# Kernel optimization log

Measured on AMD Instinct MI355X. Metric: run time of the kernel, lower is better.

The kernel has to match this reference:

```python
import jax, jax.numpy as jnp
import numpy as np
import math

LOG2PI = math.log(2 * math.pi)
K = 16           # num_comp
C = 64           # channels
S, NN, T = 2, 207, 12
NFEAT = S * NN * T  # 4968 = in_features of the Conv1d(k=1) projections


def setup_inputs() -> dict:
    key = jax.random.key(0)
    ks = jax.random.split(key, 7)
    x = jax.random.normal(ks[0], (8, C, S, NN, T), dtype=jnp.float32)
    scale = 0.02
    alpha_w = jax.random.normal(ks[1], (K, NFEAT), dtype=jnp.float32) * scale
    alpha_b = jax.random.normal(ks[2], (K,), dtype=jnp.float32) * scale
    sigma_w = jax.random.normal(ks[3], (K, NFEAT), dtype=jnp.float32) * scale
    sigma_b = jax.random.normal(ks[4], (K,), dtype=jnp.float32) * scale
    mu_w = jax.random.normal(ks[5], (K, NFEAT), dtype=jnp.float32) * scale
    mu_b = jax.random.normal(ks[6], (K,), dtype=jnp.float32) * scale
    return {"x": x, "alpha_w": alpha_w, "alpha_b": alpha_b,
            "sigma_w": sigma_w, "sigma_b": sigma_b, "mu_w": mu_w, "mu_b": mu_b}


def reference(x, alpha_w, alpha_b, sigma_w, sigma_b, mu_w, mu_b):
    b, c, s, n, t = x.shape
    hd = x.reshape(b, c, -1)                       # (b, c, N); torch's hd after final permute
    # Conv1d(kernel=1) over the (b, N, c) layout == per-(b,c) linear N -> K
    def proj(w, bias):
        return jnp.einsum('bcn,kn->bck', hd, w) + bias  # (b, c, K)
    alphas = jax.nn.softmax(proj(alpha_w, alpha_b), axis=-1)   # softmax over K
    sigma = jnp.exp(proj(sigma_w, sigma_b))                    # (b, c, K)
    mu = proj(mu_w, mu_b)                                      # (b, c, K)

    # log N(h | mu_k, sigma_k^2): (b, c, N, K) via broadcasting (original repeats)
    z = (hd[..., None] - mu[:, :, None, :]) / sigma[:, :, None, :]
    log_component_prob = -jnp.log(sigma)[:, :, None, :] - 0.5 * LOG2PI - 0.5 * z * z
    log_prob = log_component_prob + jnp.log(alphas)[:, :, None, :]
    # original computes log(sum(exp(.))) without max-subtraction; replicate exactly
    log_sum = jnp.log(jnp.sum(jnp.exp(log_prob), axis=-1, keepdims=True))
    weightedlogPdf = log_prob - log_sum                        # (b, c, N, K)
    labels = jnp.argmax(weightedlogPdf, axis=-1)               # (b, c, N) int

    # cluster_norm: due to torch aliasing (new_mu = new_sigma = labels, same storage),
    # both end up equal to sigma gathered by label, so norm uses sigma_g for center+scale.
    sigma_g = jnp.take_along_axis(sigma, labels, axis=2)       # (b, c, N)
    norm = (hd - sigma_g) / (sigma_g + 1e-5)
    out = norm.reshape(b, c, s, n, t)

    # probability regularization loss
    first_item = jnp.mean(jnp.exp(weightedlogPdf) * log_component_prob)
    q_z = jnp.mean(weightedlogPdf, axis=2)                     # (b, c, K)
    kl = jnp.mean(alphas * (jnp.log(alphas) - q_z))            # F.kl_div(q_z, alphas, 'mean')
    loss = kl - first_item
    return out, loss
```

## Files before the change

kernel.cpp:

```cpp
#include <hip/hip_runtime.h>
#include <math.h>

#define NROWS 512
#define NFEAT 4968
#define NVEC4 1242
#define HALF_LOG2PI 0.91893853320467274178032973640562

__global__ __launch_bounds__(256) void proj_kernel(
    const float* __restrict__ x,
    const float* __restrict__ aw,
    const float* __restrict__ sw,
    const float* __restrict__ mw,
    double* __restrict__ proj)
{
    const int jgroup = blockIdx.x >> 9;
    const int row    = blockIdx.x & 511;
    const int t = threadIdx.x;
    const int j = t >> 4;
    const int s = t & 15;

    const float* W = (jgroup == 0) ? aw : (jgroup == 1) ? sw : mw;
    const float4* xp = (const float4*)(x + (size_t)row * NFEAT);
    const float4* wp = (const float4*)(W + (size_t)j * NFEAT);

    double a0 = 0.0, a1 = 0.0, a2 = 0.0, a3 = 0.0;
    #pragma unroll 4
    for (int i = s; i < NVEC4; i += 16) {
        float4 xv = xp[i], wv = wp[i];
        a0 = fma((double)xv.x, (double)wv.x, a0);
        a1 = fma((double)xv.y, (double)wv.y, a1);
        a2 = fma((double)xv.z, (double)wv.z, a2);
        a3 = fma((double)xv.w, (double)wv.w, a3);
    }
    double a = (a0 + a1) + (a2 + a3);

    #pragma unroll
    for (int off = 8; off; off >>= 1) a += __shfl_xor(a, off, 16);

    if (s == 0)
        proj[(size_t)row * 48 + jgroup * 16 + j] = a;
}

__global__ __launch_bounds__(256) void gmm_kernel(
    const float* __restrict__ x,
    const double* __restrict__ proj,
    const float* __restrict__ ab,
    const float* __restrict__ sb,
    const float* __restrict__ mb,
    float* __restrict__ out,
    float* __restrict__ part_kl,
    float* __restrict__ part_fi)
{
    const int row = blockIdx.x;
    const int tid = threadIdx.x;

    __shared__ double mu_s[16], isg_s[16], cl_s[16];
    __shared__ double sig_s[16], ivp_s[16];
    __shared__ float  la_s[16], al_s[16];
    __shared__ float  red[4][18];
    __shared__ float  tot_s[18];
    __shared__ float  kl_s[16];

    if (tid < 16) {
        int k = tid;
        double pa = proj[row * 48 + k]      + (double)ab[k];
        double ps = proj[row * 48 + 16 + k] + (double)sb[k];
        double pm = proj[row * 48 + 32 + k] + (double)mb[k];

        double m = pa;
        #pragma unroll
        for (int off = 8; off; off >>= 1) m = fmax(m, __shfl_xor(m, off, 16));
        double e = exp(pa - m);
        double ss = e;
        #pragma unroll
        for (int off = 8; off; off >>= 1) ss += __shfl_xor(ss, off, 16);
        double alpha = e / ss;
        double la = log(alpha);

        double sg  = exp(ps);
        double lsg = log(sg);

        mu_s[k]  = pm;
        isg_s[k] = 1.0 / sg;
        cl_s[k]  = la - lsg - HALF_LOG2PI;
        sig_s[k] = sg;
        ivp_s[k] = 1.0 / (sg + 1e-5);
        la_s[k]  = (float)la;
        al_s[k]  = (float)alpha;
    }
    __syncthreads();

    double mu_r[16], isg_r[16], cl_r[16];
    float  la_r[16];
    #pragma unroll
    for (int k = 0; k < 16; ++k) {
        mu_r[k] = mu_s[k]; isg_r[k] = isg_s[k];
        cl_r[k] = cl_s[k]; la_r[k] = la_s[k];
    }

    float S1[16];
    #pragma unroll
    for (int k = 0; k < 16; ++k) S1[k] = 0.f;
    float S2 = 0.f;
    float FI = 0.f;

    const float* xr = x + (size_t)row * NFEAT;
    float* outr = out + (size_t)row * NFEAT;

    for (int n = tid; n < NFEAT; n += 256) {
        double h = (double)xr[n];
        double maxlp = -1.0e300;
        int lab = 0;
        float sumexp = 0.f, s1 = 0.f;
        #pragma unroll
        for (int k = 0; k < 16; ++k) {
            double z  = (h - mu_r[k]) * isg_r[k];
            double lp = fma(z * z, -0.5, cl_r[k]);
            if (lp > maxlp) { maxlp = lp; lab = k; }
            float lpf = (float)lp;
            float e   = __expf(lpf);
            float lcp = lpf - la_r[k];
            sumexp += e;
            s1 = fmaf(e, lcp, s1);
            S1[k] += lcp;
        }
        S2 += __logf(sumexp);
        FI += s1 / sumexp;

        double sg = sig_s[lab];
        outr[n] = (float)((h - sg) * ivp_s[lab]);
    }

    float vals[18];
    #pragma unroll
    for (int i = 0; i < 16; ++i) vals[i] = S1[i];
    vals[16] = S2; vals[17] = FI;

    #pragma unroll
    for (int i = 0; i < 18; ++i) {
        float v = vals[i];
        #pragma unroll
        for (int off = 32; off; off >>= 1) v += __shfl_xor(v, off, 64);
        vals[i] = v;
    }
    const int wave = tid >> 6, lane = tid & 63;
    if (lane == 0) {
        #pragma unroll
        for (int i = 0; i < 18; ++i) red[wave][i] = vals[i];
    }
    __syncthreads();
    if (tid < 18)
        tot_s[tid] = red[0][tid] + red[1][tid] + red[2][tid] + red[3][tid];
    __syncthreads();
    if (tid < 16) {
        const float invN = 1.0f / (float)NFEAT;
        float q = tot_s[tid] * invN + la_s[tid] - tot_s[16] * invN;
        kl_s[tid] = al_s[tid] * (la_s[tid] - q);
    }
    __syncthreads();
    if (tid == 0) {
        float kacc = 0.f;
        #pragma unroll
        for (int i = 0; i < 16; ++i) kacc += kl_s[i];
        part_kl[row] = kacc;
        part_fi[row] = tot_s[17];
    }
}

__global__ __launch_bounds__(256) void loss_kernel(
    const float* __restrict__ part_kl,
    const float* __restrict__ part_fi,
    float* __restrict__ loss_out)
{
    const int tid = threadIdx.x;
    double a = 0.0, b = 0.0;
    for (int i = tid; i < NROWS; i += 256) {
        a += (double)part_kl[i];
        b += (double)part_fi[i];
    }
    #pragma unroll
    for (int off = 32; off; off >>= 1) {
        a += __shfl_xor(a, off, 64);
        b += __shfl_xor(b, off, 64);
    }
    __shared__ double ra[4], rb[4];
    const int wave = tid >> 6, lane = tid & 63;
    if (lane == 0) { ra[wave] = a; rb[wave] = b; }
    __syncthreads();
    if (tid == 0) {
        double ka = ra[0] + ra[1] + ra[2] + ra[3];
        double kb = rb[0] + rb[1] + rb[2] + rb[3];
        loss_out[0] = (float)(ka / 8192.0 - kb / 40697856.0);
    }
}

extern "C" void kernel_launch(void* const* d_in, const int* in_sizes, int n_in,
                              void* d_out, int out_size, void* d_ws, size_t ws_size,
                              hipStream_t stream) {
    const float* x  = (const float*)d_in[0];
    const float* aw = (const float*)d_in[1];
    const float* ab = (const float*)d_in[2];
    const float* sw = (const float*)d_in[3];
    const float* sb = (const float*)d_in[4];
    const float* mw = (const float*)d_in[5];
    const float* mb = (const float*)d_in[6];
    float* out = (float*)d_out;

    double* proj   = (double*)d_ws;
    float* part_kl = (float*)(proj + NROWS * 48);
    float* part_fi = part_kl + NROWS;

    proj_kernel<<<3 * NROWS, 256, 0, stream>>>(x, aw, sw, mw, proj);
    gmm_kernel<<<NROWS, 256, 0, stream>>>(x, proj, ab, sb, mb, out, part_kl, part_fi);
    loss_kernel<<<1, 256, 0, stream>>>(part_kl, part_fi, out + (size_t)NROWS * NFEAT);
}
```

Before: 62.55 us.

## Tile projection over rows and K-slices, split GMM rows across blocks

```diff
diff --git a/kernel.cpp b/kernel.cpp
--- a/kernel.cpp
+++ b/kernel.cpp
@@ -4,6 +4,9 @@
 #define NROWS 512
 #define NFEAT 4968
 #define NVEC4 1242
+#define KSLICES 6
+#define SLICE4 207
+#define GSL 1242
 #define HALF_LOG2PI 0.91893853320467274178032973640562
 
 __global__ __launch_bounds__(256) void proj_kernel(
@@ -11,82 +14,110 @@
     const float* __restrict__ aw,
     const float* __restrict__ sw,
     const float* __restrict__ mw,
-    double* __restrict__ proj)
-{
-    const int jgroup = blockIdx.x >> 9;
-    const int row    = blockIdx.x & 511;
+    double* __restrict__ pp)
+{
+    const int rowtile = blockIdx.x & 63;
+    const int jg      = (blockIdx.x >> 6) % 3;
+    const int sl      = blockIdx.x / 192;
     const int t = threadIdx.x;
     const int j = t >> 4;
-    const int s = t & 15;
-
-    const float* W = (jgroup == 0) ? aw : (jgroup == 1) ? sw : mw;
-    const float4* xp = (const float4*)(x + (size_t)row * NFEAT);
-    const float4* wp = (const float4*)(W + (size_t)j * NFEAT);
-
-    double a0 = 0.0, a1 = 0.0, a2 = 0.0, a3 = 0.0;
-    #pragma unroll 4
-    for (int i = s; i < NVEC4; i += 16) {
-        float4 xv = xp[i], wv = wp[i];
-        a0 = fma((double)xv.x, (double)wv.x, a0);
-        a1 = fma((double)xv.y, (double)wv.y, a1);
-        a2 = fma((double)xv.z, (double)wv.z, a2);
-        a3 = fma((double)xv.w, (double)wv.w, a3);
-    }
-    double a = (a0 + a1) + (a2 + a3);
-
-    #pragma unroll
-    for (int off = 8; off; off >>= 1) a += __shfl_xor(a, off, 16);
-
-    if (s == 0)
-        proj[(size_t)row * 48 + jgroup * 16 + j] = a;
-}
-
-__global__ __launch_bounds__(256) void gmm_kernel(
-    const float* __restrict__ x,
-    const double* __restrict__ proj,
+    const int s16 = t & 15;
+    const int row0 = rowtile * 8;
+
+    const float* W = (jg == 0) ? aw : (jg == 1) ? sw : mw;
+    const float4* wp = (const float4*)(W + (size_t)j * NFEAT) + sl * SLICE4;
+    const float4* xp = (const float4*)(x + (size_t)row0 * NFEAT) + sl * SLICE4;
+
+    double acc[8][2];
+    #pragma unroll
+    for (int r = 0; r < 8; ++r) { acc[r][0] = 0.0; acc[r][1] = 0.0; }
+
+    for (int i = s16; i < SLICE4; i += 16) {
+        float4 wv = wp[i];
+        #pragma unroll
+        for (int r = 0; r < 8; ++r) {
+            float4 xv = xp[(size_t)r * NVEC4 + i];
+            acc[r][0] = fma((double)xv.x, (double)wv.x, acc[r][0]);
+            acc[r][0] = fma((double)xv.y, (double)wv.y, acc[r][0]);
+            acc[r][1] = fma((double)xv.z, (double)wv.z, acc[r][1]);
+            acc[r][1] = fma((double)xv.w, (double)wv.w, acc[r][1]);
+        }
+    }
+
+    #pragma unroll
+    for (int r = 0; r < 8; ++r) {
+        double a = acc[r][0] + acc[r][1];
+        #pragma unroll
+        for (int off = 8; off; off >>= 1) a += __shfl_xor(a, off, 16);
+        if (s16 == 0)
+            pp[((size_t)(row0 + r) * 48 + jg * 16 + j) * KSLICES + sl] = a;
+    }
+}
+
+__global__ __launch_bounds__(256) void params_kernel(
+    const double* __restrict__ pp,
     const float* __restrict__ ab,
     const float* __restrict__ sb,
     const float* __restrict__ mb,
+    double* __restrict__ mu, double* __restrict__ isg, double* __restrict__ cl,
+    double* __restrict__ sig, double* __restrict__ ivp,
+    float* __restrict__ la, float* __restrict__ al)
+{
+    const int g = blockIdx.x * 256 + threadIdx.x;
+    const int row = g >> 4, k = g & 15;
+    const double* p = pp + ((size_t)row * 48 + k) * KSLICES;
+
+    double pa = 0.0, ps = 0.0, pm = 0.0;
+    #pragma unroll
+    for (int s = 0; s < KSLICES; ++s) {
+        pa += p[s];
+        ps += p[16 * KSLICES + s];
+        pm += p[32 * KSLICES + s];
+    }
+    pa += (double)ab[k]; ps += (double)sb[k]; pm += (double)mb[k];
+
+    double m = pa;
+    #pragma unroll
+    for (int off = 8; off; off >>= 1) m = fmax(m, __shfl_xor(m, off, 16));
+    double e = exp(pa - m);
+    double ss = e;
+    #pragma unroll
+    for (int off = 8; off; off >>= 1) ss += __shfl_xor(ss, off, 16);
+    double alpha = e / ss;
+    double lav = log(alpha);
+
+    double sg  = exp(ps);
+    double lsg = log(sg);
+
+    mu[g]  = pm;
+    isg[g] = 1.0 / sg;
+    cl[g]  = lav - lsg - HALF_LOG2PI;
+    sig[g] = sg;
+    ivp[g] = 1.0 / (sg + 1e-5);
+    la[g]  = (float)lav;
+    al[g]  = (float)alpha;
+}
+
+__global__ __launch_bounds__(256) void gmm_kernel(
+    const float* __restrict__ x,
+    const double* __restrict__ mu, const double* __restrict__ isg,
+    const double* __restrict__ cl, const float* __restrict__ laf,
+    const double* __restrict__ sig, const double* __restrict__ ivp,
     float* __restrict__ out,
-    float* __restrict__ part_kl,
-    float* __restrict__ part_fi)
-{
-    const int row = blockIdx.x;
+    float* __restrict__ S1p, float* __restrict__ S2p, float* __restrict__ FIp)
+{
+    const int row = blockIdx.x >> 2;
+    const int sl  = blockIdx.x & 3;
     const int tid = threadIdx.x;
-
-    __shared__ double mu_s[16], isg_s[16], cl_s[16];
+    const int g0  = row * 16;
+
     __shared__ double sig_s[16], ivp_s[16];
-    __shared__ float  la_s[16], al_s[16];
     __shared__ float  red[4][18];
     __shared__ float  tot_s[18];
-    __shared__ float  kl_s[16];
 
     if (tid < 16) {
-        int k = tid;
-        double pa = proj[row * 48 + k]      + (double)ab[k];
-        double ps = proj[row * 48 + 16 + k] + (double)sb[k];
-        double pm = proj[row * 48 + 32 + k] + (double)mb[k];
-
-        double m = pa;
-        #pragma unroll
-        for (int off = 8; off; off >>= 1) m = fmax(m, __shfl_xor(m, off, 16));
-        double e = exp(pa - m);
-        double ss = e;
-        #pragma unroll
-        for (int off = 8; off; off >>= 1) ss += __shfl_xor(ss, off, 16);
-        double alpha = e / ss;
-        double la = log(alpha);
-
-        double sg  = exp(ps);
-        double lsg = log(sg);
-
-        mu_s[k]  = pm;
-        isg_s[k] = 1.0 / sg;
-        cl_s[k]  = la - lsg - HALF_LOG2PI;
-        sig_s[k] = sg;
-        ivp_s[k] = 1.0 / (sg + 1e-5);
-        la_s[k]  = (float)la;
-        al_s[k]  = (float)alpha;
+        sig_s[tid] = sig[g0 + tid];
+        ivp_s[tid] = ivp[g0 + tid];
     }
     __syncthreads();
 
@@ -94,20 +125,21 @@
     float  la_r[16];
     #pragma unroll
     for (int k = 0; k < 16; ++k) {
-        mu_r[k] = mu_s[k]; isg_r[k] = isg_s[k];
-        cl_r[k] = cl_s[k]; la_r[k] = la_s[k];
+        mu_r[k]  = mu[g0 + k];
+        isg_r[k] = isg[g0 + k];
+        cl_r[k]  = cl[g0 + k];
+        la_r[k]  = laf[g0 + k];
     }
 
     float S1[16];
     #pragma unroll
     for (int k = 0; k < 16; ++k) S1[k] = 0.f;
-    float S2 = 0.f;
-    float FI = 0.f;
-
-    const float* xr = x + (size_t)row * NFEAT;
-    float* outr = out + (size_t)row * NFEAT;
-
-    for (int n = tid; n < NFEAT; n += 256) {
+    float S2 = 0.f, FI = 0.f;
+
+    const float* xr = x + (size_t)row * NFEAT + sl * GSL;
+    float* outr = out + (size_t)row * NFEAT + sl * GSL;
+
+    for (int n = tid; n < GSL; n += 256) {
         double h = (double)xr[n];
         double maxlp = -1.0e300;
         int lab = 0;
@@ -152,45 +184,48 @@
     if (tid < 18)
         tot_s[tid] = red[0][tid] + red[1][tid] + red[2][tid] + red[3][tid];
     __syncthreads();
-    if (tid < 16) {
-        const float invN = 1.0f / (float)NFEAT;
-        float q = tot_s[tid] * invN + la_s[tid] - tot_s[16] * invN;
-        kl_s[tid] = al_s[tid] * (la_s[tid] - q);
-    }
+    if (tid < 16) S1p[(size_t)blockIdx.x * 16 + tid] = tot_s[tid];
+    if (tid == 16) S2p[blockIdx.x] = tot_s[16];
+    if (tid == 17) FIp[blockIdx.x] = tot_s[17];
+}
+
+__global__ __launch_bounds__(1024) void loss_kernel(
+    const float* __restrict__ S1p, const float* __restrict__ S2p,
+    const float* __restrict__ FIp,
+    const float* __restrict__ la, const float* __restrict__ al,
+    float* __restrict__ loss_out)
+{
+    const int tid = threadIdx.x;
+    const float invN = 1.0f / (float)NFEAT;
+
+    float kl_acc = 0.f;
+    for (int g = tid; g < 8192; g += 1024) {
+        int row = g >> 4, k = g & 15;
+        int b = row * 4;
+        float s1 = S1p[(size_t)(b + 0) * 16 + k] + S1p[(size_t)(b + 1) * 16 + k]
+                 + S1p[(size_t)(b + 2) * 16 + k] + S1p[(size_t)(b + 3) * 16 + k];
+        float s2 = S2p[b + 0] + S2p[b + 1] + S2p[b + 2] + S2p[b + 3];
+        float lav = la[g], alv = al[g];
+        float q = s1 * invN + lav - s2 * invN;
+        kl_acc += alv * (lav - q);
+    }
+    float fi_acc = 0.f;
+    for (int i = tid; i < 2048; i += 1024) fi_acc += FIp[i];
+
+    #pragma unroll
+    for (int off = 32; off; off >>= 1) {
+        kl_acc += __shfl_xor(kl_acc, off, 64);
+        fi_acc += __shfl_xor(fi_acc, off, 64);
+    }
+    __shared__ float ra[16], rb[16];
+    const int wave = tid >> 6, lane = tid & 63;
+    if (lane == 0) { ra[wave] = kl_acc; rb[wave] = fi_acc; }
     __syncthreads();
     if (tid == 0) {
-        float kacc = 0.f;
-        #pragma unroll
-        for (int i = 0; i < 16; ++i) kacc += kl_s[i];
-        part_kl[row] = kacc;
-        part_fi[row] = tot_s[17];
-    }
-}
-
-__global__ __launch_bounds__(256) void loss_kernel(
-    const float* __restrict__ part_kl,
-    const float* __restrict__ part_fi,
-    float* __restrict__ loss_out)
-{
-    const int tid = threadIdx.x;
-    double a = 0.0, b = 0.0;
-    for (int i = tid; i < NROWS; i += 256) {
-        a += (double)part_kl[i];
-        b += (double)part_fi[i];
-    }
-    #pragma unroll
-    for (int off = 32; off; off >>= 1) {
-        a += __shfl_xor(a, off, 64);
-        b += __shfl_xor(b, off, 64);
-    }
-    __shared__ double ra[4], rb[4];
-    const int wave = tid >> 6, lane = tid & 63;
-    if (lane == 0) { ra[wave] = a; rb[wave] = b; }
-    __syncthreads();
-    if (tid == 0) {
-        double ka = ra[0] + ra[1] + ra[2] + ra[3];
-        double kb = rb[0] + rb[1] + rb[2] + rb[3];
-        loss_out[0] = (float)(ka / 8192.0 - kb / 40697856.0);
+        float ka = 0.f, kb = 0.f;
+        #pragma unroll
+        for (int i = 0; i < 16; ++i) { ka += ra[i]; kb += rb[i]; }
+        loss_out[0] = ka / 8192.0f - kb / 40697856.0f;
     }
 }
 
@@ -206,11 +241,22 @@
     const float* mb = (const float*)d_in[6];
     float* out = (float*)d_out;
 
-    double* proj   = (double*)d_ws;
-    float* part_kl = (float*)(proj + NROWS * 48);
-    float* part_fi = part_kl + NROWS;
-
-    proj_kernel<<<3 * NROWS, 256, 0, stream>>>(x, aw, sw, mw, proj);
-    gmm_kernel<<<NROWS, 256, 0, stream>>>(x, proj, ab, sb, mb, out, part_kl, part_fi);
-    loss_kernel<<<1, 256, 0, stream>>>(part_kl, part_fi, out + (size_t)NROWS * NFEAT);
-}
+    double* pp  = (double*)d_ws;
+    double* mu  = pp + (size_t)NROWS * 48 * KSLICES;
+    double* isg = mu + 8192;
+    double* cl  = isg + 8192;
+    double* sig = cl + 8192;
+    double* ivp = sig + 8192;
+    float* la   = (float*)(ivp + 8192);
+    float* al   = la + 8192;
+    float* S1p  = al + 8192;
+    float* S2p  = S1p + 2048 * 16;
+    float* FIp  = S2p + 2048;
+
+    proj_kernel<<<64 * 3 * KSLICES, 256, 0, stream>>>(x, aw, sw, mw, pp);
+    params_kernel<<<32, 256, 0, stream>>>(pp, ab, sb, mb, mu, isg, cl, sig, ivp, la, al);
+    gmm_kernel<<<NROWS * 4, 256, 0, stream>>>(x, mu, isg, cl, la, sig, ivp,
+                                              out, S1p, S2p, FIp);
+    loss_kernel<<<1, 1024, 0, stream>>>(S1p, S2p, FIp, la, al,
+                                        out + (size_t)NROWS * NFEAT);
+}
```

After: 58.18 us. -7.0%, faster.
